# Kernel tuning notes

Hardware: AMD Instinct MI355X
Metric: run time of the kernel (lower is better)

The kernel has to match this reference:

```python
import jax, jax.numpy as jnp
import numpy as np

EPS = 1e-06


def setup_inputs() -> dict:
    key = jax.random.key(0)
    ks = jax.random.split(key, 6)
    B, L, N = 64, 4096, 128
    F = L // 2 + 1  # 2049 rfft bins
    E = 8
    x = jax.random.normal(ks[0], (B, L, N), dtype=jnp.float32)
    band_boundaries = jax.random.normal(ks[1], (E - 1,), dtype=jnp.float32)
    # gate: Linear(F,F) -> ReLU -> Linear(F,E); stored as [in,out] matrices
    gate_w1 = jax.random.normal(ks[2], (F, F), dtype=jnp.float32) * (1.0 / np.sqrt(F))
    gate_b1 = jnp.zeros((F,), dtype=jnp.float32)
    gate_w2 = jax.random.normal(ks[3], (F, E), dtype=jnp.float32) * (1.0 / np.sqrt(F))
    gate_b2 = jnp.zeros((E,), dtype=jnp.float32)
    return {"x": x, "band_boundaries": band_boundaries,
            "gate_w1": gate_w1, "gate_b1": gate_b1,
            "gate_w2": gate_w2, "gate_b2": gate_b2}


def reference(x, band_boundaries, gate_w1, gate_b1, gate_w2, gate_b2):
    # FrequencyMoE forward (residual_add=True). x: [B, L, N]
    B, L, N = x.shape
    F = L // 2 + 1
    xN = jnp.transpose(x, (0, 2, 1))  # [B, N, L]
    mean = jnp.mean(xN, axis=-1, keepdims=True)
    var = jnp.var(xN, axis=-1, keepdims=True) + EPS
    # NOTE: original code computes x_norm then overwrites with xN (normalization skipped),
    # but still rescales the reconstruction by sqrt(var) and adds mean back. Faithful copy.
    freq = jnp.fft.rfft(xN, n=L, axis=-1)  # [B, N, F] complex64

    # learnable band boundaries -> integer bin indices (non-differentiable, as in torch .long())
    bb = jnp.sort(jax.nn.sigmoid(band_boundaries))
    b01 = jnp.concatenate([jnp.zeros((1,), bb.dtype), bb, jnp.ones((1,), bb.dtype)])
    idx = jnp.clip((b01 * F).astype(jnp.int32), 0, F)
    idx = idx.at[-1].set(F)  # [E+1]

    bins = jnp.arange(F)
    # per-expert frequency masks [E, F]: bin in [idx[e], idx[e+1])
    masks = ((bins[None, :] >= idx[:-1, None]) & (bins[None, :] < idx[1:, None])).astype(xN.dtype)

    # gating on mean magnitude spectrum over variables
    mag = jnp.mean(jnp.abs(freq), axis=1)  # [B, F]
    h = jax.nn.relu(mag @ gate_w1 + gate_b1)
    weights = jax.nn.softmax(h @ gate_w2 + gate_b2, axis=-1)  # [B, E]

    # fused weighted-mask combination: sum_e w[b,e]*mask[e,f] applied to spectrum
    wmask = weights @ masks  # [B, F]
    freq_out = freq * wmask[:, None, :]
    x_rec = jnp.fft.irfft(freq_out, n=L, axis=-1)  # [B, N, L]
    x_rec = x_rec * jnp.sqrt(var) + mean
    outN = xN + x_rec  # residual_add=True
    return jnp.transpose(outN, (0, 2, 1))  # [B, L, N]
```

## Files before the change

kernel.cpp:

```cpp
#include <hip/hip_runtime.h>

#define B_ 64
#define L_ 4096
#define N_ 128
#define F_ 2049
#define M_ 2048

__device__ __forceinline__ int pidx(int a) { return a + (a >> 3); }

__device__ __forceinline__ float2 cadd(float2 a, float2 b) { return make_float2(a.x + b.x, a.y + b.y); }
__device__ __forceinline__ float2 csub(float2 a, float2 b) { return make_float2(a.x - b.x, a.y - b.y); }
__device__ __forceinline__ float2 cmul(float2 a, float2 b) {
  return make_float2(a.x * b.x - a.y * b.y, a.x * b.y + a.y * b.x);
}
template <int SGN>
__device__ __forceinline__ float2 mulsi(float2 a) {
  return (SGN > 0) ? make_float2(-a.y, a.x) : make_float2(a.y, -a.x);
}

template <int SGN>
__device__ __forceinline__ void dft8(float2* v) {
  const float C = 0.70710678118654752f;
  float2 t0 = cadd(v[0], v[4]), t1 = csub(v[0], v[4]);
  float2 t2 = cadd(v[2], v[6]), t3 = mulsi<SGN>(csub(v[2], v[6]));
  float2 t4 = cadd(v[1], v[5]), t5 = csub(v[1], v[5]);
  float2 t6 = cadd(v[3], v[7]), t7 = mulsi<SGN>(csub(v[3], v[7]));
  float2 u0 = cadd(t0, t2), u1 = csub(t0, t2);
  float2 u2 = cadd(t1, t3), u3 = csub(t1, t3);
  float2 u4 = cadd(t4, t6), u5 = csub(t4, t6);
  float2 u6 = cadd(t5, t7), u7 = csub(t5, t7);
  float2 w1 = make_float2(C, (SGN > 0) ? C : -C);
  float2 w3 = make_float2(-C, (SGN > 0) ? C : -C);
  float2 a5 = mulsi<SGN>(u5);
  float2 b6 = cmul(u6, w1);
  float2 b7 = cmul(u7, w3);
  v[0] = cadd(u0, u4); v[4] = csub(u0, u4);
  v[2] = cadd(u1, a5); v[6] = csub(u1, a5);
  v[1] = cadd(u2, b6); v[5] = csub(u2, b6);
  v[3] = cadd(u3, b7); v[7] = csub(u3, b7);
}

template <int SGN>
__device__ __forceinline__ void dft4(float2* v) {
  float2 e0 = cadd(v[0], v[2]), e1 = csub(v[0], v[2]);
  float2 o0 = cadd(v[1], v[3]), o1 = mulsi<SGN>(csub(v[1], v[3]));
  v[0] = cadd(e0, o0); v[2] = csub(e0, o0);
  v[1] = cadd(e1, o1); v[3] = csub(e1, o1);
}

template <int SGN>
__device__ __forceinline__ float2 twroot(int pm) {
  float ang = (float)pm * 0.00306796157577128245f;
  float sv, cv;
  __sincosf(ang, &sv, &cv);
  return make_float2(cv, (SGN > 0) ? sv : -sv);
}
__device__ __forceinline__ void tw8w(float2* v, float2 w) {
  float2 wk = w;
  v[1] = cmul(v[1], wk);
#pragma unroll
  for (int k = 2; k < 8; ++k) { wk = cmul(wk, w); v[k] = cmul(v[k], wk); }
}
template <int SGN>
__device__ __forceinline__ void tw8(float2* v, int pm) { tw8w(v, twroot<SGN>(pm)); }

template <int SGN>
__device__ __forceinline__ void fft2048(float2* __restrict__ buf, float2* v, int t) {
  dft8<SGN>(v);
  tw8<SGN>(v, t);
  __syncthreads();
#pragma unroll
  for (int k = 0; k < 8; ++k) buf[pidx(8 * t + k)] = v[k];
  __syncthreads();
#pragma unroll
  for (int r = 0; r < 8; ++r) v[r] = buf[pidx(t + 256 * r)];
  dft8<SGN>(v);
  tw8<SGN>(v, t & ~7);
  __syncthreads();
  {
    int q = t & 7, p = t >> 3;
#pragma unroll
    for (int k = 0; k < 8; ++k) buf[pidx(q + 8 * (8 * p + k))] = v[k];
  }
  __syncthreads();
#pragma unroll
  for (int r = 0; r < 8; ++r) v[r] = buf[pidx(t + 256 * r)];
  dft8<SGN>(v);
  tw8<SGN>(v, t & ~63);
  __syncthreads();
  {
    int q = t & 63, p = t >> 6;
#pragma unroll
    for (int k = 0; k < 8; ++k) buf[pidx(q + 64 * (8 * p + k))] = v[k];
  }
  __syncthreads();
  float2 w0[4], w1s[4];
#pragma unroll
  for (int r = 0; r < 4; ++r) {
    w0[r] = buf[pidx(t + 512 * r)];
    w1s[r] = buf[pidx(t + 256 + 512 * r)];
  }
  dft4<SGN>(w0);
  dft4<SGN>(w1s);
  __syncthreads();
#pragma unroll
  for (int k = 0; k < 4; ++k) {
    buf[pidx(t + 512 * k)] = w0[k];
    buf[pidx(t + 256 + 512 * k)] = w1s[k];
  }
  __syncthreads();
}

template <int SGN>
__device__ __forceinline__ void fft2048x2(float2* __restrict__ bufA, float2* __restrict__ bufB,
                                          float2* va, float2* vb, int t) {
  dft8<SGN>(va); dft8<SGN>(vb);
  { float2 w = twroot<SGN>(t); tw8w(va, w); tw8w(vb, w); }
  __syncthreads();
#pragma unroll
  for (int k = 0; k < 8; ++k) { bufA[pidx(8 * t + k)] = va[k]; bufB[pidx(8 * t + k)] = vb[k]; }
  __syncthreads();
#pragma unroll
  for (int r = 0; r < 8; ++r) { va[r] = bufA[pidx(t + 256 * r)]; vb[r] = bufB[pidx(t + 256 * r)]; }
  dft8<SGN>(va); dft8<SGN>(vb);
  { float2 w = twroot<SGN>(t & ~7); tw8w(va, w); tw8w(vb, w); }
  __syncthreads();
  {
    int q = t & 7, p = t >> 3;
#pragma unroll
    for (int k = 0; k < 8; ++k) {
      int a = pidx(q + 8 * (8 * p + k));
      bufA[a] = va[k]; bufB[a] = vb[k];
    }
  }
  __syncthreads();
#pragma unroll
  for (int r = 0; r < 8; ++r) { va[r] = bufA[pidx(t + 256 * r)]; vb[r] = bufB[pidx(t + 256 * r)]; }
  dft8<SGN>(va); dft8<SGN>(vb);
  { float2 w = twroot<SGN>(t & ~63); tw8w(va, w); tw8w(vb, w); }
  __syncthreads();
  {
    int q = t & 63, p = t >> 6;
#pragma unroll
    for (int k = 0; k < 8; ++k) {
      int a = pidx(q + 64 * (8 * p + k));
      bufA[a] = va[k]; bufB[a] = vb[k];
    }
  }
  __syncthreads();
  float2 wA0[4], wA1[4], wB0[4], wB1[4];
#pragma unroll
  for (int r = 0; r < 4; ++r) {
    wA0[r] = bufA[pidx(t + 512 * r)];
    wA1[r] = bufA[pidx(t + 256 + 512 * r)];
    wB0[r] = bufB[pidx(t + 512 * r)];
    wB1[r] = bufB[pidx(t + 256 + 512 * r)];
  }
  dft4<SGN>(wA0); dft4<SGN>(wA1); dft4<SGN>(wB0); dft4<SGN>(wB1);
  __syncthreads();
#pragma unroll
  for (int k = 0; k < 4; ++k) {
    bufA[pidx(t + 512 * k)] = wA0[k];
    bufA[pidx(t + 256 + 512 * k)] = wA1[k];
    bufB[pidx(t + 512 * k)] = wB0[k];
    bufB[pidx(t + 256 + 512 * k)] = wB1[k];
  }
  __syncthreads();
}

__global__ __launch_bounds__(256) void transpose4_k(const float* __restrict__ in,
                                                    float* __restrict__ out,
                                                    int R, int C) {
  __shared__ float tile[64][65];
  const float* ip = in + (size_t)blockIdx.z * R * C;
  float* op = out + (size_t)blockIdx.z * R * C;
  int c0 = blockIdx.x * 64;
  int r0 = blockIdx.y * 64;
  int t = threadIdx.x;
  {
    int fx = t & 15;
    int rq = t >> 4;
#pragma unroll
    for (int i = 0; i < 4; ++i) {
      int r = rq + 16 * i;
      float4 v = *(const float4*)&ip[(size_t)(r0 + r) * C + (c0 + 4 * fx)];
      tile[r][4 * fx + 0] = v.x;
      tile[r][4 * fx + 1] = v.y;
      tile[r][4 * fx + 2] = v.z;
      tile[r][4 * fx + 3] = v.w;
    }
  }
  __syncthreads();
  {
    int gm = t & 15;
    int cq = t >> 4;
#pragma unroll
    for (int i = 0; i < 4; ++i) {
      int c = cq + 16 * i;
      float4 v;
      v.x = tile[4 * gm + 0][c];
      v.y = tile[4 * gm + 1][c];
      v.z = tile[4 * gm + 2][c];
      v.w = tile[4 * gm + 3][c];
      *(float4*)&op[(size_t)(c0 + c) * R + (r0 + 4 * gm)] = v;
    }
  }
}

template <int S>
__global__ __launch_bounds__(256) void p1_fft_mag(const float* __restrict__ src,
                                                  float* __restrict__ magsum) {
  __shared__ float2 buf[2304];
  int t = threadIdx.x;
  int blk = blockIdx.x;
  int b = blk >> 7;
  int n = blk & 127;
  const float* base = (S == 1) ? (src + (size_t)blk * L_)
                               : (src + (size_t)b * L_ * N_ + n);
  float2 v[8];
  if (S == 1) {
    const float2* r2 = (const float2*)base;
#pragma unroll
    for (int r = 0; r < 8; ++r) v[r] = r2[t + 256 * r];
  } else {
#pragma unroll
    for (int r = 0; r < 8; ++r) {
      int k = t + 256 * r;
      v[r] = make_float2(base[(size_t)(2 * k) * S], base[(size_t)(2 * k + 1) * S]);
    }
  }
  fft2048<-1>(buf, v, t);

  float* msum = magsum + (size_t)b * F_;
#pragma unroll
  for (int i = 0; i < 8; ++i) {
    int f = t + 256 * i;
    float mg;
    if (f == 0) {
      float2 z = buf[pidx(0)];
      mg = fabsf(z.x + z.y);
      atomicAdd(&msum[2048], fabsf(z.x - z.y));
    } else {
      float2 zf = buf[pidx(f)], zm = buf[pidx(2048 - f)];
      float Are = 0.5f * (zf.x + zm.x), Aim = 0.5f * (zf.y - zm.y);
      float Bre = 0.5f * (zf.y + zm.y), Bim = -0.5f * (zf.x - zm.x);
      float ang = (float)f * 0.00153398078788564117f;
      float sv, cv;
      __sincosf(ang, &sv, &cv);
      float Xre = Are + cv * Bre + sv * Bim;
      float Xim = Aim + cv * Bim - sv * Bre;
      mg = sqrtf(Xre * Xre + Xim * Xim);
    }
    atomicAdd(&msum[f], mg);
  }
}

__global__ __launch_bounds__(256, 4) void p1_fft_mag_z2(const float* __restrict__ src,
                                                        float2* __restrict__ zout,
                                                        float* __restrict__ magsum) {
  __shared__ float2 bufA[2304];
  __shared__ float2 bufB[2304];
  int t = threadIdx.x;
  int blk = blockIdx.x;
  int b = blk >> 6;
  const float2* rA = (const float2*)(src + (size_t)(2 * blk) * L_);
  const float2* rB = rA + M_;
  float2 va[8], vb[8];
#pragma unroll
  for (int r = 0; r < 8; ++r) { va[r] = rA[t + 256 * r]; vb[r] = rB[t + 256 * r]; }
  fft2048x2<-1>(bufA, bufB, va, vb, t);

  float* msum = magsum + (size_t)b * F_;
  float2* zrA = zout + (size_t)(2 * blk) * (size_t)M_;
  float2* zrB = zrA + M_;
#pragma unroll
  for (int i = 0; i < 4; ++i) {
    int f = t + 256 * i;
    if (f == 0) {
      float2 zA = bufA[pidx(0)], zcA = bufA[pidx(1024)];
      float2 zB = bufB[pidx(0)], zcB = bufB[pidx(1024)];
      zrA[0] = zA; zrA[1024] = zcA;
      zrB[0] = zB; zrB[1024] = zcB;
      atomicAdd(&msum[0], fabsf(zA.x + zA.y) + fabsf(zB.x + zB.y));
      atomicAdd(&msum[2048], fabsf(zA.x - zA.y) + fabsf(zB.x - zB.y));
      atomicAdd(&msum[1024], sqrtf(zcA.x * zcA.x + zcA.y * zcA.y) +
                             sqrtf(zcB.x * zcB.x + zcB.y * zcB.y));
    } else {
      float2 zfA = bufA[pidx(f)], zmA = bufA[pidx(2048 - f)];
      float2 zfB = bufB[pidx(f)], zmB = bufB[pidx(2048 - f)];
      zrA[f] = zfA; zrA[2048 - f] = zmA;
      zrB[f] = zfB; zrB[2048 - f] = zmB;
      float ang = (float)f * 0.00153398078788564117f;
      float sv, cv;
      __sincosf(ang, &sv, &cv);
      float Are = 0.5f * (zfA.x + zmA.x), Aim = 0.5f * (zfA.y - zmA.y);
      float Bre = 0.5f * (zfA.y + zmA.y), Bim = -0.5f * (zfA.x - zmA.x);
      float WBre = cv * Bre + sv * Bim;
      float WBim = cv * Bim - sv * Bre;
      float XreA = Are + WBre, XimA = Aim + WBim;
      float XmreA = Are - WBre, XmimA = Aim - WBim;
      float Cre = 0.5f * (zfB.x + zmB.x), Cim = 0.5f * (zfB.y - zmB.y);
      float Dre = 0.5f * (zfB.y + zmB.y), Dim = -0.5f * (zfB.x - zmB.x);
      float WDre = cv * Dre + sv * Dim;
      float WDim = cv * Dim - sv * Dre;
      float XreB = Cre + WDre, XimB = Cim + WDim;
      float XmreB = Cre - WDre, XmimB = Cim - WDim;
      atomicAdd(&msum[f], sqrtf(XreA * XreA + XimA * XimA) +
                          sqrtf(XreB * XreB + XimB * XimB));
      atomicAdd(&msum[2048 - f], sqrtf(XmreA * XmreA + XmimA * XmimA) +
                                 sqrtf(XmreB * XmreB + XmimB * XmimB));
    }
  }
}

__global__ __launch_bounds__(256) void magt_k(const float* __restrict__ mag,
                                              float* __restrict__ magT) {
  int idx = blockIdx.x * 256 + threadIdx.x;
  if (idx >= 64 * F_) return;
  int f = idx >> 6, b = idx & 63;
  magT[idx] = mag[(size_t)b * F_ + f] * (1.0f / 128.0f);
}

#define G1K 33
__global__ __launch_bounds__(256) void g1_gemm(const float* __restrict__ magT,
                                               const float* __restrict__ W1,
                                               float* __restrict__ hsum) {
  int o = blockIdx.x * 256 + threadIdx.x;
  if (o >= F_) return;
  int i0 = blockIdx.y * G1K;
  int i1 = min(F_, i0 + G1K);
  float acc[64];
#pragma unroll
  for (int b = 0; b < 64; ++b) acc[b] = 0.f;
  for (int i = i0; i < i1; ++i) {
    float w = W1[(size_t)i * F_ + o];
    const float* mrow = magT + (size_t)i * 64;
#pragma unroll
    for (int b = 0; b < 64; ++b) acc[b] = fmaf(mrow[b], w, acc[b]);
  }
#pragma unroll
  for (int b = 0; b < 64; ++b) atomicAdd(&hsum[(size_t)b * F_ + o], acc[b]);
}

__global__ __launch_bounds__(256) void g2_gate(const float* __restrict__ hsum,
                                               const float* __restrict__ gb1,
                                               const float* __restrict__ W2,
                                               const float* __restrict__ gb2,
                                               const float* __restrict__ bbs,
                                               float* __restrict__ wmask) {
  __shared__ float red[256 * 8];
  __shared__ float wsm[8];
  __shared__ int idxs[9];
  int b = blockIdx.x;
  int t = threadIdx.x;
  float p[8];
#pragma unroll
  for (int e = 0; e < 8; ++e) p[e] = 0.f;
  for (int o = t; o < F_; o += 256) {
    float hv = hsum[(size_t)b * F_ + o] + gb1[o];
    hv = fmaxf(hv, 0.f);
    const float4* w2p = (const float4*)(W2 + (size_t)o * 8);
    float4 wa = w2p[0], wb = w2p[1];
    p[0] += hv * wa.x; p[1] += hv * wa.y; p[2] += hv * wa.z; p[3] += hv * wa.w;
    p[4] += hv * wb.x; p[5] += hv * wb.y; p[6] += hv * wb.z; p[7] += hv * wb.w;
  }
#pragma unroll
  for (int e = 0; e < 8; ++e) red[t * 8 + e] = p[e];
  __syncthreads();
  for (int s = 128; s >= 1; s >>= 1) {
    if (t < s) {
#pragma unroll
      for (int e = 0; e < 8; ++e) red[t * 8 + e] += red[(t + s) * 8 + e];
    }
    __syncthreads();
  }
  if (t == 0) {
    float lg[8];
    float mx = -1e30f;
#pragma unroll
    for (int e = 0; e < 8; ++e) { lg[e] = red[e] + gb2[e]; mx = fmaxf(mx, lg[e]); }
    float sm = 0.f;
#pragma unroll
    for (int e = 0; e < 8; ++e) { lg[e] = expf(lg[e] - mx); sm += lg[e]; }
    float inv = 1.f / sm;
#pragma unroll
    for (int e = 0; e < 8; ++e) wsm[e] = lg[e] * inv;
    float bv[7];
#pragma unroll
    for (int k = 0; k < 7; ++k) bv[k] = 1.f / (1.f + expf(-bbs[k]));
    for (int a = 1; a < 7; ++a) {
      float v = bv[a];
      int j = a - 1;
      while (j >= 0 && bv[j] > v) { bv[j + 1] = bv[j]; --j; }
      bv[j + 1] = v;
    }
    idxs[0] = 0;
    idxs[8] = F_;
    for (int k = 0; k < 7; ++k) {
      int v = (int)(bv[k] * (float)F_);
      v = min(max(v, 0), F_);
      idxs[k + 1] = v;
    }
  }
  __syncthreads();
  for (int f = t; f < F_; f += 256) {
    float wv = 0.f;
#pragma unroll
    for (int e = 0; e < 8; ++e)
      if (f >= idxs[e] && f < idxs[e + 1]) wv = wsm[e];
    wmask[(size_t)b * F_ + f] = wv;
  }
}

__device__ __forceinline__ void filter_pair(float2& zf, float2& zm, int f,
                                            float cv, float sv,
                                            float mf, float mg) {
  float Are = 0.5f * (zf.x + zm.x), Aim = 0.5f * (zf.y - zm.y);
  float Bre = 0.5f * (zf.y + zm.y), Bim = -0.5f * (zf.x - zm.x);
  float WBre = cv * Bre + sv * Bim;
  float WBim = cv * Bim - sv * Bre;
  float Xre = Are + WBre, Xim = Aim + WBim;
  float Xmre = Are - WBre, Xmim = -(Aim - WBim);
  Xre *= mf; Xim *= mf;
  Xmre *= mg; Xmim *= mg;
  float Apre = 0.5f * (Xre + Xmre), Apim = 0.5f * (Xim - Xmim);
  float Tre = 0.5f * (Xre - Xmre), Tim = 0.5f * (Xim + Xmim);
  float Bpre = cv * Tre - sv * Tim;
  float Bpim = cv * Tim + sv * Tre;
  zf = make_float2(Apre - Bpim, Apim + Bpre);
  float Agre = 0.5f * (Xmre + Xre), Agim = 0.5f * (Xmim - Xim);
  float Tgre = 0.5f * (Xmre - Xre), Tgim = 0.5f * (Xmim + Xim);
  float Bgre = -(cv * Tgre + sv * Tgim);
  float Bgim = -(cv * Tgim - sv * Tgre);
  zm = make_float2(Agre - Bgim, Agim + Bgre);
}

__global__ __launch_bounds__(256, 4) void p3_filter_z2(float2* __restrict__ zbuf,
                                                       const float* __restrict__ wmask) {
  __shared__ float2 bufA[2304];
  __shared__ float2 bufB[2304];
  __shared__ float rb[16];
  __shared__ float sstat[4];
  int t = threadIdx.x;
  int blk = blockIdx.x;
  int b = blk >> 6;
  float2* zrA = zbuf + (size_t)(2 * blk) * (size_t)M_;
  float2* zrB = zrA + M_;
  float2 va[8], vb[8];
  float lsqA = 0.f, lsqB = 0.f;
#pragma unroll
  for (int r = 0; r < 8; ++r) {
    float2 zA = zrA[t + 256 * r];
    float2 zB = zrB[t + 256 * r];
    va[r] = zA; vb[r] = zB;
    lsqA += zA.x * zA.x + zA.y * zA.y;
    lsqB += zB.x * zB.x + zB.y * zB.y;
  }
#pragma unroll
  for (int r = 0; r < 8; ++r) {
    bufA[pidx(t + 256 * r)] = va[r];
    bufB[pidx(t + 256 * r)] = vb[r];
  }
  for (int off = 32; off > 0; off >>= 1) {
    lsqA += __shfl_down(lsqA, off);
    lsqB += __shfl_down(lsqB, off);
  }
  {
    int lane = t & 63, wid = t >> 6;
    if (lane == 0) { rb[wid] = lsqA; rb[8 + wid] = lsqB; }
  }
  __syncthreads();
  if (t < 2) {
    const float* rr = rb + 8 * t;
    float s2 = rr[0] + rr[1] + rr[2] + rr[3];
    float2 z0 = (t == 0) ? bufA[pidx(0)] : bufB[pidx(0)];
    float mean = (z0.x + z0.y) * (1.0f / 4096.0f);
    float sumsq = s2 * (1.0f / 2048.0f);
    float var = sumsq * (1.0f / 4096.0f) - mean * mean + 1e-6f;
    sstat[2 * t] = mean;
    sstat[2 * t + 1] = sqrtf(var);
  }
  __syncthreads();

  float meanA = sstat[0], sdvA = sstat[1];
  float meanB = sstat[2], sdvB = sstat[3];
  const float* wm = wmask + (size_t)b * F_;

#pragma unroll
  for (int i = 0; i < 4; ++i) {
    int f = t + 256 * i;
    if (f == 0) {
      float w0 = wm[0], wN = wm[2048], wC = wm[1024];
      {
        float2 z0 = bufA[pidx(0)], zc = bufA[pidx(1024)];
        float X0 = (z0.x + z0.y) * (1.f + sdvA * w0);
        float XM = (z0.x - z0.y) * (1.f + sdvA * wN);
        bufA[pidx(0)] = make_float2(0.5f * (X0 + XM), 0.5f * (X0 - XM));
        float mc = 1.f + sdvA * wC;
        bufA[pidx(1024)] = make_float2(zc.x * mc, zc.y * mc);
      }
      {
        float2 z0 = bufB[pidx(0)], zc = bufB[pidx(1024)];
        float X0 = (z0.x + z0.y) * (1.f + sdvB * w0);
        float XM = (z0.x - z0.y) * (1.f + sdvB * wN);
        bufB[pidx(0)] = make_float2(0.5f * (X0 + XM), 0.5f * (X0 - XM));
        float mc = 1.f + sdvB * wC;
        bufB[pidx(1024)] = make_float2(zc.x * mc, zc.y * mc);
      }
    } else {
      float ang = (float)f * 0.00153398078788564117f;
      float sv, cv;
      __sincosf(ang, &sv, &cv);
      float wf = wm[f], wg = wm[2048 - f];
      {
        float2 zf = bufA[pidx(f)], zm = bufA[pidx(2048 - f)];
        filter_pair(zf, zm, f, cv, sv, 1.f + sdvA * wf, 1.f + sdvA * wg);
        bufA[pidx(f)] = zf; bufA[pidx(2048 - f)] = zm;
      }
      {
        float2 zf = bufB[pidx(f)], zm = bufB[pidx(2048 - f)];
        filter_pair(zf, zm, f, cv, sv, 1.f + sdvB * wf, 1.f + sdvB * wg);
        bufB[pidx(f)] = zf; bufB[pidx(2048 - f)] = zm;
      }
    }
  }
  __syncthreads();
#pragma unroll
  for (int r = 0; r < 8; ++r) {
    va[r] = bufA[pidx(t + 256 * r)];
    vb[r] = bufB[pidx(t + 256 * r)];
  }
  fft2048x2<1>(bufA, bufB, va, vb, t);

  const float inv = 1.0f / 2048.0f;
#pragma unroll
  for (int r = 0; r < 8; ++r) {
    int k = t + 256 * r;
    float2 zA = bufA[pidx(k)];
    float2 zB = bufB[pidx(k)];
    zrA[k] = make_float2(zA.x * inv + meanA, zA.y * inv + meanA);
    zrB[k] = make_float2(zB.x * inv + meanB, zB.y * inv + meanB);
  }
}

template <int S>
__global__ __launch_bounds__(256) void p3_filter(const float* __restrict__ src,
                                                 const float* __restrict__ wmask,
                                                 float* __restrict__ dstp) {
  __shared__ float2 buf[2304];
  __shared__ float sstat[2];
  int t = threadIdx.x;
  int blk = blockIdx.x;
  int b = blk >> 7;
  int n = blk & 127;
  const float* base = (S == 1) ? (src + (size_t)blk * L_)
                               : (src + (size_t)b * L_ * N_ + n);
  float* obase = (S == 1) ? (dstp + (size_t)blk * L_)
                          : (dstp + (size_t)b * L_ * N_ + n);
  float2 v[8];
  float lsum = 0.f, lsq = 0.f;
  if (S == 1) {
    const float2* r2 = (const float2*)base;
#pragma unroll
    for (int r = 0; r < 8; ++r) {
      float2 z = r2[t + 256 * r];
      v[r] = z;
      lsum += z.x + z.y;
      lsq += z.x * z.x + z.y * z.y;
    }
  } else {
#pragma unroll
    for (int r = 0; r < 8; ++r) {
      int k = t + 256 * r;
      float2 z = make_float2(base[(size_t)(2 * k) * S], base[(size_t)(2 * k + 1) * S]);
      v[r] = z;
      lsum += z.x + z.y;
      lsq += z.x * z.x + z.y * z.y;
    }
  }
  for (int off = 32; off > 0; off >>= 1) {
    lsum += __shfl_down(lsum, off);
    lsq += __shfl_down(lsq, off);
  }
  {
    float* rb = (float*)buf;
    int lane = t & 63, wid = t >> 6;
    if (lane == 0) { rb[wid] = lsum; rb[8 + wid] = lsq; }
    __syncthreads();
    if (t == 0) {
      float s1 = rb[0] + rb[1] + rb[2] + rb[3];
      float s2 = rb[8] + rb[9] + rb[10] + rb[11];
      float mean = s1 * (1.0f / 4096.0f);
      float var = s2 * (1.0f / 4096.0f) - mean * mean + 1e-6f;
      sstat[0] = mean;
      sstat[1] = sqrtf(var);
    }
  }
  fft2048<-1>(buf, v, t);

  float mean = sstat[0], sdv = sstat[1];
  const float* wm = wmask + (size_t)b * F_;

#pragma unroll
  for (int i = 0; i < 4; ++i) {
    int f = t + 256 * i;
    if (f == 0) {
      float2 z0 = buf[pidx(0)];
      float2 zc = buf[pidx(1024)];
      float X0 = (z0.x + z0.y) * (1.f + sdv * wm[0]);
      float XM = (z0.x - z0.y) * (1.f + sdv * wm[2048]);
      buf[pidx(0)] = make_float2(0.5f * (X0 + XM), 0.5f * (X0 - XM));
      float mc = 1.f + sdv * wm[1024];
      buf[pidx(1024)] = make_float2(zc.x * mc, zc.y * mc);
    } else {
      float ang = (float)f * 0.00153398078788564117f;
      float sv, cv;
      __sincosf(ang, &sv, &cv);
      float2 zf = buf[pidx(f)], zm = buf[pidx(2048 - f)];
      filter_pair(zf, zm, f, cv, sv, 1.f + sdv * wm[f], 1.f + sdv * wm[2048 - f]);
      buf[pidx(f)] = zf; buf[pidx(2048 - f)] = zm;
    }
  }
  __syncthreads();
#pragma unroll
  for (int r = 0; r < 8; ++r) v[r] = buf[pidx(t + 256 * r)];
  fft2048<1>(buf, v, t);

  const float inv = 1.0f / 2048.0f;
  if (S == 1) {
    float2* o2 = (float2*)obase;
#pragma unroll
    for (int r = 0; r < 8; ++r) {
      int k = t + 256 * r;
      float2 z = buf[pidx(k)];
      o2[k] = make_float2(z.x * inv + mean, z.y * inv + mean);
    }
  } else {
#pragma unroll
    for (int r = 0; r < 8; ++r) {
      int k = t + 256 * r;
      float2 z = buf[pidx(k)];
      obase[(size_t)(2 * k) * S] = z.x * inv + mean;
      obase[(size_t)(2 * k + 1) * S] = z.y * inv + mean;
    }
  }
}

extern "C" void kernel_launch(void* const* d_in, const int* in_sizes, int n_in,
                              void* d_out, int out_size, void* d_ws,
                              size_t ws_size, hipStream_t stream) {
  const float* x = (const float*)d_in[0];
  const float* bbs = (const float*)d_in[1];
  const float* W1 = (const float*)d_in[2];
  const float* gb1 = (const float*)d_in[3];
  const float* W2 = (const float*)d_in[4];
  const float* gb2 = (const float*)d_in[5];
  float* out = (float*)d_out;

  const size_t bigElems = (size_t)B_ * N_ * L_;
  const size_t smallBytes = (size_t)3 * B_ * F_ * sizeof(float);
  const bool fast = ws_size >= bigElems * sizeof(float) + smallBytes;

  char* smallBase = (char*)d_ws + (fast ? bigElems * sizeof(float) : 0);
  float* magsum = (float*)smallBase;
  float* hsum = magsum + (size_t)B_ * F_;
  float* wmaskp = hsum + (size_t)B_ * F_;

  hipMemsetAsync(magsum, 0, (size_t)2 * B_ * F_ * sizeof(float), stream);

  const int g1x = (F_ + 255) / 256;
  const int g1y = (F_ + G1K - 1) / G1K;
  const int mtb = (64 * F_ + 255) / 256;
  if (fast) {
    float2* Z = (float2*)d_ws;
    transpose4_k<<<dim3(N_ / 64, L_ / 64, B_), 256, 0, stream>>>(x, out, L_, N_);
    p1_fft_mag_z2<<<dim3(B_ * N_ / 2), 256, 0, stream>>>(out, Z, magsum);
    magt_k<<<dim3(mtb), 256, 0, stream>>>(magsum, wmaskp);
    g1_gemm<<<dim3(g1x, g1y), 256, 0, stream>>>(wmaskp, W1, hsum);
    g2_gate<<<dim3(B_), 256, 0, stream>>>(hsum, gb1, W2, gb2, bbs, wmaskp);
    p3_filter_z2<<<dim3(B_ * N_ / 2), 256, 0, stream>>>(Z, wmaskp);
    transpose4_k<<<dim3(L_ / 64, N_ / 64, B_), 256, 0, stream>>>((float*)d_ws, out, N_, L_);
  } else {
    p1_fft_mag<N_><<<dim3(B_ * N_), 256, 0, stream>>>(x, magsum);
    magt_k<<<dim3(mtb), 256, 0, stream>>>(magsum, wmaskp);
    g1_gemm<<<dim3(g1x, g1y), 256, 0, stream>>>(wmaskp, W1, hsum);
    g2_gate<<<dim3(B_), 256, 0, stream>>>(hsum, gb1, W2, gb2, bbs, wmaskp);
    p3_filter<N_><<<dim3(B_ * N_), 256, 0, stream>>>(x, wmaskp, out);
  }
}
```

Measured before the change: 473.8 us.

## Batch four packed FFTs per block and write transposed magnitudes directly

The forward and inverse FFT kernels now process four packed 2048-point complex FFTs per block instead of two, sharing twiddles, sincos and mask loads across more rows. The magnitude pass also reduces across the four rows before each atomic and writes into the transposed, pre-scaled [F,B] layout, so the separate magt_k transpose kernel is dropped from the fast path. The cost is doubled shared memory (about 74 KB) and more registers per block, with launch bounds lowered to two blocks per SM, which may reduce occupancy.

```diff
diff --git a/kernel.cpp b/kernel.cpp
--- a/kernel.cpp
+++ b/kernel.cpp
@@ -112,58 +112,85 @@
 }
 
 template <int SGN>
-__device__ __forceinline__ void fft2048x2(float2* __restrict__ bufA, float2* __restrict__ bufB,
-                                          float2* va, float2* vb, int t) {
-  dft8<SGN>(va); dft8<SGN>(vb);
-  { float2 w = twroot<SGN>(t); tw8w(va, w); tw8w(vb, w); }
-  __syncthreads();
-#pragma unroll
-  for (int k = 0; k < 8; ++k) { bufA[pidx(8 * t + k)] = va[k]; bufB[pidx(8 * t + k)] = vb[k]; }
-  __syncthreads();
-#pragma unroll
-  for (int r = 0; r < 8; ++r) { va[r] = bufA[pidx(t + 256 * r)]; vb[r] = bufB[pidx(t + 256 * r)]; }
-  dft8<SGN>(va); dft8<SGN>(vb);
-  { float2 w = twroot<SGN>(t & ~7); tw8w(va, w); tw8w(vb, w); }
+__device__ __forceinline__ void fft2048x4(float2 (*__restrict__ buf)[2304],
+                                          float2 (*__restrict__ v)[8], int t) {
+#pragma unroll
+  for (int j = 0; j < 4; ++j) dft8<SGN>(v[j]);
+  {
+    float2 w = twroot<SGN>(t);
+#pragma unroll
+    for (int j = 0; j < 4; ++j) tw8w(v[j], w);
+  }
+  __syncthreads();
+#pragma unroll
+  for (int k = 0; k < 8; ++k) {
+    int a = pidx(8 * t + k);
+#pragma unroll
+    for (int j = 0; j < 4; ++j) buf[j][a] = v[j][k];
+  }
+  __syncthreads();
+#pragma unroll
+  for (int r = 0; r < 8; ++r) {
+    int a = pidx(t + 256 * r);
+#pragma unroll
+    for (int j = 0; j < 4; ++j) v[j][r] = buf[j][a];
+  }
+#pragma unroll
+  for (int j = 0; j < 4; ++j) dft8<SGN>(v[j]);
+  {
+    float2 w = twroot<SGN>(t & ~7);
+#pragma unroll
+    for (int j = 0; j < 4; ++j) tw8w(v[j], w);
+  }
   __syncthreads();
   {
     int q = t & 7, p = t >> 3;
 #pragma unroll
     for (int k = 0; k < 8; ++k) {
       int a = pidx(q + 8 * (8 * p + k));
-      bufA[a] = va[k]; bufB[a] = vb[k];
-    }
-  }
-  __syncthreads();
-#pragma unroll
-  for (int r = 0; r < 8; ++r) { va[r] = bufA[pidx(t + 256 * r)]; vb[r] = bufB[pidx(t + 256 * r)]; }
-  dft8<SGN>(va); dft8<SGN>(vb);
-  { float2 w = twroot<SGN>(t & ~63); tw8w(va, w); tw8w(vb, w); }
+#pragma unroll
+      for (int j = 0; j < 4; ++j) buf[j][a] = v[j][k];
+    }
+  }
+  __syncthreads();
+#pragma unroll
+  for (int r = 0; r < 8; ++r) {
+    int a = pidx(t + 256 * r);
+#pragma unroll
+    for (int j = 0; j < 4; ++j) v[j][r] = buf[j][a];
+  }
+#pragma unroll
+  for (int j = 0; j < 4; ++j) dft8<SGN>(v[j]);
+  {
+    float2 w = twroot<SGN>(t & ~63);
+#pragma unroll
+    for (int j = 0; j < 4; ++j) tw8w(v[j], w);
+  }
   __syncthreads();
   {
     int q = t & 63, p = t >> 6;
 #pragma unroll
     for (int k = 0; k < 8; ++k) {
       int a = pidx(q + 64 * (8 * p + k));
-      bufA[a] = va[k]; bufB[a] = vb[k];
-    }
-  }
-  __syncthreads();
-  float2 wA0[4], wA1[4], wB0[4], wB1[4];
+#pragma unroll
+      for (int j = 0; j < 4; ++j) buf[j][a] = v[j][k];
+    }
+  }
+  __syncthreads();
 #pragma unroll
   for (int r = 0; r < 4; ++r) {
-    wA0[r] = bufA[pidx(t + 512 * r)];
-    wA1[r] = bufA[pidx(t + 256 + 512 * r)];
-    wB0[r] = bufB[pidx(t + 512 * r)];
-    wB1[r] = bufB[pidx(t + 256 + 512 * r)];
-  }
-  dft4<SGN>(wA0); dft4<SGN>(wA1); dft4<SGN>(wB0); dft4<SGN>(wB1);
+    int a0 = pidx(t + 512 * r), a1 = pidx(t + 256 + 512 * r);
+#pragma unroll
+    for (int j = 0; j < 4; ++j) { v[j][r] = buf[j][a0]; v[j][4 + r] = buf[j][a1]; }
+  }
+#pragma unroll
+  for (int j = 0; j < 4; ++j) { dft4<SGN>(v[j]); dft4<SGN>(v[j] + 4); }
   __syncthreads();
 #pragma unroll
   for (int k = 0; k < 4; ++k) {
-    bufA[pidx(t + 512 * k)] = wA0[k];
-    bufA[pidx(t + 256 + 512 * k)] = wA1[k];
-    bufB[pidx(t + 512 * k)] = wB0[k];
-    bufB[pidx(t + 256 + 512 * k)] = wB1[k];
+    int a0 = pidx(t + 512 * k), a1 = pidx(t + 256 + 512 * k);
+#pragma unroll
+    for (int j = 0; j < 4; ++j) { buf[j][a0] = v[j][k]; buf[j][a1] = v[j][4 + k]; }
   }
   __syncthreads();
 }
@@ -255,60 +282,62 @@
   }
 }
 
-__global__ __launch_bounds__(256, 4) void p1_fft_mag_z2(const float* __restrict__ src,
+__global__ __launch_bounds__(256, 2) void p1_fft_mag_z4(const float* __restrict__ src,
                                                         float2* __restrict__ zout,
-                                                        float* __restrict__ magsum) {
-  __shared__ float2 bufA[2304];
-  __shared__ float2 bufB[2304];
+                                                        float* __restrict__ magT) {
+  __shared__ float2 buf[4][2304];
   int t = threadIdx.x;
   int blk = blockIdx.x;
-  int b = blk >> 6;
-  const float2* rA = (const float2*)(src + (size_t)(2 * blk) * L_);
-  const float2* rB = rA + M_;
-  float2 va[8], vb[8];
-#pragma unroll
-  for (int r = 0; r < 8; ++r) { va[r] = rA[t + 256 * r]; vb[r] = rB[t + 256 * r]; }
-  fft2048x2<-1>(bufA, bufB, va, vb, t);
-
-  float* msum = magsum + (size_t)b * F_;
-  float2* zrA = zout + (size_t)(2 * blk) * (size_t)M_;
-  float2* zrB = zrA + M_;
+  int b = blk >> 5;
+  const float2* r0 = (const float2*)(src + (size_t)(4 * blk) * L_);
+  float2 v[4][8];
+#pragma unroll
+  for (int r = 0; r < 8; ++r) {
+#pragma unroll
+    for (int j = 0; j < 4; ++j) v[j][r] = r0[j * M_ + t + 256 * r];
+  }
+  fft2048x4<-1>(buf, v, t);
+
+  float2* zr = zout + (size_t)(4 * blk) * (size_t)M_;
+  const float sc = 1.0f / 128.0f;
 #pragma unroll
   for (int i = 0; i < 4; ++i) {
     int f = t + 256 * i;
     if (f == 0) {
-      float2 zA = bufA[pidx(0)], zcA = bufA[pidx(1024)];
-      float2 zB = bufB[pidx(0)], zcB = bufB[pidx(1024)];
-      zrA[0] = zA; zrA[1024] = zcA;
-      zrB[0] = zB; zrB[1024] = zcB;
-      atomicAdd(&msum[0], fabsf(zA.x + zA.y) + fabsf(zB.x + zB.y));
-      atomicAdd(&msum[2048], fabsf(zA.x - zA.y) + fabsf(zB.x - zB.y));
-      atomicAdd(&msum[1024], sqrtf(zcA.x * zcA.x + zcA.y * zcA.y) +
-                             sqrtf(zcB.x * zcB.x + zcB.y * zcB.y));
+      float s0 = 0.f, sN = 0.f, sC = 0.f;
+#pragma unroll
+      for (int j = 0; j < 4; ++j) {
+        float2 z = buf[j][pidx(0)], zc = buf[j][pidx(1024)];
+        zr[j * M_ + 0] = z;
+        zr[j * M_ + 1024] = zc;
+        s0 += fabsf(z.x + z.y);
+        sN += fabsf(z.x - z.y);
+        sC += sqrtf(zc.x * zc.x + zc.y * zc.y);
+      }
+      atomicAdd(&magT[0 * 64 + b], s0 * sc);
+      atomicAdd(&magT[2048 * 64 + b], sN * sc);
+      atomicAdd(&magT[1024 * 64 + b], sC * sc);
     } else {
-      float2 zfA = bufA[pidx(f)], zmA = bufA[pidx(2048 - f)];
-      float2 zfB = bufB[pidx(f)], zmB = bufB[pidx(2048 - f)];
-      zrA[f] = zfA; zrA[2048 - f] = zmA;
-      zrB[f] = zfB; zrB[2048 - f] = zmB;
       float ang = (float)f * 0.00153398078788564117f;
       float sv, cv;
       __sincosf(ang, &sv, &cv);
-      float Are = 0.5f * (zfA.x + zmA.x), Aim = 0.5f * (zfA.y - zmA.y);
-      float Bre = 0.5f * (zfA.y + zmA.y), Bim = -0.5f * (zfA.x - zmA.x);
-      float WBre = cv * Bre + sv * Bim;
-      float WBim = cv * Bim - sv * Bre;
-      float XreA = Are + WBre, XimA = Aim + WBim;
-      float XmreA = Are - WBre, XmimA = Aim - WBim;
-      float Cre = 0.5f * (zfB.x + zmB.x), Cim = 0.5f * (zfB.y - zmB.y);
-      float Dre = 0.5f * (zfB.y + zmB.y), Dim = -0.5f * (zfB.x - zmB.x);
-      float WDre = cv * Dre + sv * Dim;
-      float WDim = cv * Dim - sv * Dre;
-      float XreB = Cre + WDre, XimB = Cim + WDim;
-      float XmreB = Cre - WDre, XmimB = Cim - WDim;
-      atomicAdd(&msum[f], sqrtf(XreA * XreA + XimA * XimA) +
-                          sqrtf(XreB * XreB + XimB * XimB));
-      atomicAdd(&msum[2048 - f], sqrtf(XmreA * XmreA + XmimA * XmimA) +
-                                 sqrtf(XmreB * XmreB + XmimB * XmimB));
+      float sf = 0.f, sg = 0.f;
+#pragma unroll
+      for (int j = 0; j < 4; ++j) {
+        float2 zf = buf[j][pidx(f)], zm = buf[j][pidx(2048 - f)];
+        zr[j * M_ + f] = zf;
+        zr[j * M_ + 2048 - f] = zm;
+        float Are = 0.5f * (zf.x + zm.x), Aim = 0.5f * (zf.y - zm.y);
+        float Bre = 0.5f * (zf.y + zm.y), Bim = -0.5f * (zf.x - zm.x);
+        float WBre = cv * Bre + sv * Bim;
+        float WBim = cv * Bim - sv * Bre;
+        float Xre = Are + WBre, Xim = Aim + WBim;
+        float Xmre = Are - WBre, Xmim = Aim - WBim;
+        sf += sqrtf(Xre * Xre + Xim * Xim);
+        sg += sqrtf(Xmre * Xmre + Xmim * Xmim);
+      }
+      atomicAdd(&magT[(size_t)f * 64 + b], sf * sc);
+      atomicAdd(&magT[(size_t)(2048 - f) * 64 + b], sg * sc);
     }
   }
 }
@@ -435,45 +464,47 @@
   zm = make_float2(Agre - Bgim, Agim + Bgre);
 }
 
-__global__ __launch_bounds__(256, 4) void p3_filter_z2(float2* __restrict__ zbuf,
+__global__ __launch_bounds__(256, 2) void p3_filter_z4(float2* __restrict__ zbuf,
                                                        const float* __restrict__ wmask) {
-  __shared__ float2 bufA[2304];
-  __shared__ float2 bufB[2304];
+  __shared__ float2 buf[4][2304];
   __shared__ float rb[16];
-  __shared__ float sstat[4];
+  __shared__ float sstat[8];
   int t = threadIdx.x;
   int blk = blockIdx.x;
-  int b = blk >> 6;
-  float2* zrA = zbuf + (size_t)(2 * blk) * (size_t)M_;
-  float2* zrB = zrA + M_;
-  float2 va[8], vb[8];
-  float lsqA = 0.f, lsqB = 0.f;
+  int b = blk >> 5;
+  float2* zr = zbuf + (size_t)(4 * blk) * (size_t)M_;
+  float2 v[4][8];
+  float lsq[4] = {0.f, 0.f, 0.f, 0.f};
 #pragma unroll
   for (int r = 0; r < 8; ++r) {
-    float2 zA = zrA[t + 256 * r];
-    float2 zB = zrB[t + 256 * r];
-    va[r] = zA; vb[r] = zB;
-    lsqA += zA.x * zA.x + zA.y * zA.y;
-    lsqB += zB.x * zB.x + zB.y * zB.y;
+#pragma unroll
+    for (int j = 0; j < 4; ++j) {
+      float2 z = zr[j * M_ + t + 256 * r];
+      v[j][r] = z;
+      lsq[j] += z.x * z.x + z.y * z.y;
+    }
   }
 #pragma unroll
   for (int r = 0; r < 8; ++r) {
-    bufA[pidx(t + 256 * r)] = va[r];
-    bufB[pidx(t + 256 * r)] = vb[r];
+    int a = pidx(t + 256 * r);
+#pragma unroll
+    for (int j = 0; j < 4; ++j) buf[j][a] = v[j][r];
   }
   for (int off = 32; off > 0; off >>= 1) {
-    lsqA += __shfl_down(lsqA, off);
-    lsqB += __shfl_down(lsqB, off);
+#pragma unroll
+    for (int j = 0; j < 4; ++j) lsq[j] += __shfl_down(lsq[j], off);
   }
   {
     int lane = t & 63, wid = t >> 6;
-    if (lane == 0) { rb[wid] = lsqA; rb[8 + wid] = lsqB; }
-  }
-  __syncthreads();
-  if (t < 2) {
-    const float* rr = rb + 8 * t;
-    float s2 = rr[0] + rr[1] + rr[2] + rr[3];
-    float2 z0 = (t == 0) ? bufA[pidx(0)] : bufB[pidx(0)];
+    if (lane == 0) {
+#pragma unroll
+      for (int j = 0; j < 4; ++j) rb[j * 4 + wid] = lsq[j];
+    }
+  }
+  __syncthreads();
+  if (t < 4) {
+    float s2 = rb[t * 4 + 0] + rb[t * 4 + 1] + rb[t * 4 + 2] + rb[t * 4 + 3];
+    float2 z0 = buf[t][pidx(0)];
     float mean = (z0.x + z0.y) * (1.0f / 4096.0f);
     float sumsq = s2 * (1.0f / 2048.0f);
     float var = sumsq * (1.0f / 4096.0f) - mean * mean + 1e-6f;
@@ -482,8 +513,6 @@
   }
   __syncthreads();
 
-  float meanA = sstat[0], sdvA = sstat[1];
-  float meanB = sstat[2], sdvB = sstat[3];
   const float* wm = wmask + (size_t)b * F_;
 
 #pragma unroll
@@ -491,55 +520,50 @@
     int f = t + 256 * i;
     if (f == 0) {
       float w0 = wm[0], wN = wm[2048], wC = wm[1024];
-      {
-        float2 z0 = bufA[pidx(0)], zc = bufA[pidx(1024)];
-        float X0 = (z0.x + z0.y) * (1.f + sdvA * w0);
-        float XM = (z0.x - z0.y) * (1.f + sdvA * wN);
-        bufA[pidx(0)] = make_float2(0.5f * (X0 + XM), 0.5f * (X0 - XM));
-        float mc = 1.f + sdvA * wC;
-        bufA[pidx(1024)] = make_float2(zc.x * mc, zc.y * mc);
-      }
-      {
-        float2 z0 = bufB[pidx(0)], zc = bufB[pidx(1024)];
-        float X0 = (z0.x + z0.y) * (1.f + sdvB * w0);
-        float XM = (z0.x - z0.y) * (1.f + sdvB * wN);
-        bufB[pidx(0)] = make_float2(0.5f * (X0 + XM), 0.5f * (X0 - XM));
-        float mc = 1.f + sdvB * wC;
-        bufB[pidx(1024)] = make_float2(zc.x * mc, zc.y * mc);
+#pragma unroll
+      for (int j = 0; j < 4; ++j) {
+        float sdv = sstat[2 * j + 1];
+        float2 z0 = buf[j][pidx(0)], zc = buf[j][pidx(1024)];
+        float X0 = (z0.x + z0.y) * (1.f + sdv * w0);
+        float XM = (z0.x - z0.y) * (1.f + sdv * wN);
+        buf[j][pidx(0)] = make_float2(0.5f * (X0 + XM), 0.5f * (X0 - XM));
+        float mc = 1.f + sdv * wC;
+        buf[j][pidx(1024)] = make_float2(zc.x * mc, zc.y * mc);
       }
     } else {
       float ang = (float)f * 0.00153398078788564117f;
       float sv, cv;
       __sincosf(ang, &sv, &cv);
       float wf = wm[f], wg = wm[2048 - f];
-      {
-        float2 zf = bufA[pidx(f)], zm = bufA[pidx(2048 - f)];
-        filter_pair(zf, zm, f, cv, sv, 1.f + sdvA * wf, 1.f + sdvA * wg);
-        bufA[pidx(f)] = zf; bufA[pidx(2048 - f)] = zm;
+#pragma unroll
+      for (int j = 0; j < 4; ++j) {
+        float sdv = sstat[2 * j + 1];
+        float2 zf = buf[j][pidx(f)], zm = buf[j][pidx(2048 - f)];
+        filter_pair(zf, zm, f, cv, sv, 1.f + sdv * wf, 1.f + sdv * wg);
+        buf[j][pidx(f)] = zf;
+        buf[j][pidx(2048 - f)] = zm;
       }
-      {
-        float2 zf = bufB[pidx(f)], zm = bufB[pidx(2048 - f)];
-        filter_pair(zf, zm, f, cv, sv, 1.f + sdvB * wf, 1.f + sdvB * wg);
-        bufB[pidx(f)] = zf; bufB[pidx(2048 - f)] = zm;
-      }
     }
   }
   __syncthreads();
 #pragma unroll
   for (int r = 0; r < 8; ++r) {
-    va[r] = bufA[pidx(t + 256 * r)];
-    vb[r] = bufB[pidx(t + 256 * r)];
-  }
-  fft2048x2<1>(bufA, bufB, va, vb, t);
+    int a = pidx(t + 256 * r);
+#pragma unroll
+    for (int j = 0; j < 4; ++j) v[j][r] = buf[j][a];
+  }
+  fft2048x4<1>(buf, v, t);
 
   const float inv = 1.0f / 2048.0f;
 #pragma unroll
   for (int r = 0; r < 8; ++r) {
     int k = t + 256 * r;
-    float2 zA = bufA[pidx(k)];
-    float2 zB = bufB[pidx(k)];
-    zrA[k] = make_float2(zA.x * inv + meanA, zA.y * inv + meanA);
-    zrB[k] = make_float2(zB.x * inv + meanB, zB.y * inv + meanB);
+#pragma unroll
+    for (int j = 0; j < 4; ++j) {
+      float mean = sstat[2 * j];
+      float2 z = buf[j][pidx(k)];
+      zr[j * M_ + k] = make_float2(z.x * inv + mean, z.y * inv + mean);
+    }
   }
 }
 
@@ -662,11 +686,11 @@
   const bool fast = ws_size >= bigElems * sizeof(float) + smallBytes;
 
   char* smallBase = (char*)d_ws + (fast ? bigElems * sizeof(float) : 0);
-  float* magsum = (float*)smallBase;
-  float* hsum = magsum + (size_t)B_ * F_;
+  float* magTp = (float*)smallBase;
+  float* hsum = magTp + (size_t)B_ * F_;
   float* wmaskp = hsum + (size_t)B_ * F_;
 
-  hipMemsetAsync(magsum, 0, (size_t)2 * B_ * F_ * sizeof(float), stream);
+  hipMemsetAsync(magTp, 0, (size_t)2 * B_ * F_ * sizeof(float), stream);
 
   const int g1x = (F_ + 255) / 256;
   const int g1y = (F_ + G1K - 1) / G1K;
@@ -674,15 +698,14 @@
   if (fast) {
     float2* Z = (float2*)d_ws;
     transpose4_k<<<dim3(N_ / 64, L_ / 64, B_), 256, 0, stream>>>(x, out, L_, N_);
-    p1_fft_mag_z2<<<dim3(B_ * N_ / 2), 256, 0, stream>>>(out, Z, magsum);
-    magt_k<<<dim3(mtb), 256, 0, stream>>>(magsum, wmaskp);
-    g1_gemm<<<dim3(g1x, g1y), 256, 0, stream>>>(wmaskp, W1, hsum);
+    p1_fft_mag_z4<<<dim3(B_ * N_ / 4), 256, 0, stream>>>(out, Z, magTp);
+    g1_gemm<<<dim3(g1x, g1y), 256, 0, stream>>>(magTp, W1, hsum);
     g2_gate<<<dim3(B_), 256, 0, stream>>>(hsum, gb1, W2, gb2, bbs, wmaskp);
-    p3_filter_z2<<<dim3(B_ * N_ / 2), 256, 0, stream>>>(Z, wmaskp);
+    p3_filter_z4<<<dim3(B_ * N_ / 4), 256, 0, stream>>>(Z, wmaskp);
     transpose4_k<<<dim3(L_ / 64, N_ / 64, B_), 256, 0, stream>>>((float*)d_ws, out, N_, L_);
   } else {
-    p1_fft_mag<N_><<<dim3(B_ * N_), 256, 0, stream>>>(x, magsum);
-    magt_k<<<dim3(mtb), 256, 0, stream>>>(magsum, wmaskp);
+    p1_fft_mag<N_><<<dim3(B_ * N_), 256, 0, stream>>>(x, magTp);
+    magt_k<<<dim3(mtb), 256, 0, stream>>>(magTp, wmaskp);
     g1_gemm<<<dim3(g1x, g1y), 256, 0, stream>>>(wmaskp, W1, hsum);
     g2_gate<<<dim3(B_), 256, 0, stream>>>(hsum, gb1, W2, gb2, bbs, wmaskp);
     p3_filter<N_><<<dim3(B_ * N_), 256, 0, stream>>>(x, wmaskp, out);
```

New measurement: 651.3 us. 1.37x slower.

## Fuse input transpose and magnitude transpose into the forward FFT kernel

Applied to the files above, without the earlier changes.

The forward FFT kernel now reads x directly in its [B,L,N] layout, gathering two adjacent variables per block with strided float2 loads. This removes the separate transpose kernel and its full round trip of the 128 MB input through memory. Magnitudes are also accumulated directly in the transposed, pre-scaled layout, which removes the magt_k kernel. A block-index swizzle spreads concurrent blocks across batches to reduce atomic contention. The trade-off is that the strided column reads use only 8 bytes per 512-byte row and so may be poorly coalesced.

```diff
diff --git a/kernel.cpp b/kernel.cpp
--- a/kernel.cpp
+++ b/kernel.cpp
@@ -255,24 +255,31 @@
   }
 }
 
-__global__ __launch_bounds__(256, 4) void p1_fft_mag_z2(const float* __restrict__ src,
-                                                        float2* __restrict__ zout,
-                                                        float* __restrict__ magsum) {
+__global__ __launch_bounds__(256, 4) void p1_fused_z2(const float* __restrict__ x,
+                                                      float2* __restrict__ zout,
+                                                      float* __restrict__ magT) {
   __shared__ float2 bufA[2304];
   __shared__ float2 bufB[2304];
   int t = threadIdx.x;
-  int blk = blockIdx.x;
+  int u = blockIdx.x;
+  int blk = (u & 7) * 512 + (u >> 3);
   int b = blk >> 6;
-  const float2* rA = (const float2*)(src + (size_t)(2 * blk) * L_);
-  const float2* rB = rA + M_;
+  int np = blk & 63;
+  const float* xb = x + (size_t)b * L_ * N_ + 2 * np;
   float2 va[8], vb[8];
 #pragma unroll
-  for (int r = 0; r < 8; ++r) { va[r] = rA[t + 256 * r]; vb[r] = rB[t + 256 * r]; }
+  for (int r = 0; r < 8; ++r) {
+    int k = t + 256 * r;
+    float2 e = *(const float2*)&xb[(size_t)(2 * k) * N_];
+    float2 o = *(const float2*)&xb[(size_t)(2 * k + 1) * N_];
+    va[r] = make_float2(e.x, o.x);
+    vb[r] = make_float2(e.y, o.y);
+  }
   fft2048x2<-1>(bufA, bufB, va, vb, t);
 
-  float* msum = magsum + (size_t)b * F_;
-  float2* zrA = zout + (size_t)(2 * blk) * (size_t)M_;
+  float2* zrA = zout + (size_t)(b * N_ + 2 * np) * (size_t)M_;
   float2* zrB = zrA + M_;
+  const float sc = 1.0f / 128.0f;
 #pragma unroll
   for (int i = 0; i < 4; ++i) {
     int f = t + 256 * i;
@@ -281,10 +288,10 @@
       float2 zB = bufB[pidx(0)], zcB = bufB[pidx(1024)];
       zrA[0] = zA; zrA[1024] = zcA;
       zrB[0] = zB; zrB[1024] = zcB;
-      atomicAdd(&msum[0], fabsf(zA.x + zA.y) + fabsf(zB.x + zB.y));
-      atomicAdd(&msum[2048], fabsf(zA.x - zA.y) + fabsf(zB.x - zB.y));
-      atomicAdd(&msum[1024], sqrtf(zcA.x * zcA.x + zcA.y * zcA.y) +
-                             sqrtf(zcB.x * zcB.x + zcB.y * zcB.y));
+      atomicAdd(&magT[0 * 64 + b], (fabsf(zA.x + zA.y) + fabsf(zB.x + zB.y)) * sc);
+      atomicAdd(&magT[2048 * 64 + b], (fabsf(zA.x - zA.y) + fabsf(zB.x - zB.y)) * sc);
+      atomicAdd(&magT[1024 * 64 + b], (sqrtf(zcA.x * zcA.x + zcA.y * zcA.y) +
+                                       sqrtf(zcB.x * zcB.x + zcB.y * zcB.y)) * sc);
     } else {
       float2 zfA = bufA[pidx(f)], zmA = bufA[pidx(2048 - f)];
       float2 zfB = bufB[pidx(f)], zmB = bufB[pidx(2048 - f)];
@@ -305,10 +312,10 @@
       float WDim = cv * Dim - sv * Dre;
       float XreB = Cre + WDre, XimB = Cim + WDim;
       float XmreB = Cre - WDre, XmimB = Cim - WDim;
-      atomicAdd(&msum[f], sqrtf(XreA * XreA + XimA * XimA) +
-                          sqrtf(XreB * XreB + XimB * XimB));
-      atomicAdd(&msum[2048 - f], sqrtf(XmreA * XmreA + XmimA * XmimA) +
-                                 sqrtf(XmreB * XmreB + XmimB * XmimB));
+      atomicAdd(&magT[(size_t)f * 64 + b],
+                (sqrtf(XreA * XreA + XimA * XimA) + sqrtf(XreB * XreB + XimB * XimB)) * sc);
+      atomicAdd(&magT[(size_t)(2048 - f) * 64 + b],
+                (sqrtf(XmreA * XmreA + XmimA * XmimA) + sqrtf(XmreB * XmreB + XmimB * XmimB)) * sc);
     }
   }
 }
@@ -662,27 +669,25 @@
   const bool fast = ws_size >= bigElems * sizeof(float) + smallBytes;
 
   char* smallBase = (char*)d_ws + (fast ? bigElems * sizeof(float) : 0);
-  float* magsum = (float*)smallBase;
-  float* hsum = magsum + (size_t)B_ * F_;
+  float* magTp = (float*)smallBase;
+  float* hsum = magTp + (size_t)B_ * F_;
   float* wmaskp = hsum + (size_t)B_ * F_;
 
-  hipMemsetAsync(magsum, 0, (size_t)2 * B_ * F_ * sizeof(float), stream);
+  hipMemsetAsync(magTp, 0, (size_t)2 * B_ * F_ * sizeof(float), stream);
 
   const int g1x = (F_ + 255) / 256;
   const int g1y = (F_ + G1K - 1) / G1K;
   const int mtb = (64 * F_ + 255) / 256;
   if (fast) {
     float2* Z = (float2*)d_ws;
-    transpose4_k<<<dim3(N_ / 64, L_ / 64, B_), 256, 0, stream>>>(x, out, L_, N_);
-    p1_fft_mag_z2<<<dim3(B_ * N_ / 2), 256, 0, stream>>>(out, Z, magsum);
-    magt_k<<<dim3(mtb), 256, 0, stream>>>(magsum, wmaskp);
-    g1_gemm<<<dim3(g1x, g1y), 256, 0, stream>>>(wmaskp, W1, hsum);
+    p1_fused_z2<<<dim3(B_ * N_ / 2), 256, 0, stream>>>(x, Z, magTp);
+    g1_gemm<<<dim3(g1x, g1y), 256, 0, stream>>>(magTp, W1, hsum);
     g2_gate<<<dim3(B_), 256, 0, stream>>>(hsum, gb1, W2, gb2, bbs, wmaskp);
     p3_filter_z2<<<dim3(B_ * N_ / 2), 256, 0, stream>>>(Z, wmaskp);
     transpose4_k<<<dim3(L_ / 64, N_ / 64, B_), 256, 0, stream>>>((float*)d_ws, out, N_, L_);
   } else {
-    p1_fft_mag<N_><<<dim3(B_ * N_), 256, 0, stream>>>(x, magsum);
-    magt_k<<<dim3(mtb), 256, 0, stream>>>(magsum, wmaskp);
+    p1_fft_mag<N_><<<dim3(B_ * N_), 256, 0, stream>>>(x, magTp);
+    magt_k<<<dim3(mtb), 256, 0, stream>>>(magTp, wmaskp);
     g1_gemm<<<dim3(g1x, g1y), 256, 0, stream>>>(wmaskp, W1, hsum);
     g2_gate<<<dim3(B_), 256, 0, stream>>>(hsum, gb1, W2, gb2, bbs, wmaskp);
     p3_filter<N_><<<dim3(B_ * N_), 256, 0, stream>>>(x, wmaskp, out);
```

Result: slower. 771.0 us (+62.7%).
